# Kernel tuning notes

Measured on AMD Instinct MI355X. Metric: run time of the kernel, lower is better.

The kernel has to match this reference:

```python
import jax, jax.numpy as jnp
import numpy as np

B, N, C, H, K = 4, 16384, 256, 8, 64
D = C // H
EPS = 1e-8

def setup_inputs() -> dict:
    key = jax.random.key(0)
    ks = jax.random.split(key, 6)
    scale = 0.02
    return {
        "voxel_features": jax.random.normal(ks[0], (B, N, C), dtype=jnp.float32),
        "cluster_assignments": jax.random.uniform(ks[1], (B, N, K), dtype=jnp.float32),
        "w_qkv": jax.random.normal(ks[2], (C, 3 * C), dtype=jnp.float32) * scale,
        "w_proj": jax.random.normal(ks[3], (C, C), dtype=jnp.float32) * scale,
        "b_proj": jnp.zeros((C,), dtype=jnp.float32),
        "cluster_bias": jax.random.normal(ks[4], (K, K), dtype=jnp.float32) * scale,
    }

def reference(voxel_features, cluster_assignments, w_qkv, w_proj, b_proj, cluster_bias):
    b, n, c = voxel_features.shape
    h, d = H, c // H
    A = cluster_assignments                                  # (B,N,K)
    qkv = (voxel_features @ w_qkv).reshape(b, n, 3, h, d)    # (B,N,3,H,D)
    q = jnp.moveaxis(qkv[:, :, 0], 1, 2)                     # (B,H,N,D)
    k = jnp.moveaxis(qkv[:, :, 1], 1, 2)
    v = jnp.moveaxis(qkv[:, :, 2], 1, 2)
    # cluster mass per (batch, cluster)
    denom = A.sum(axis=1) + EPS                              # (B,K)
    # cluster-pooled K/V: contraction over N (the huge broadcast-sum in torch)
    k_cluster = jnp.einsum('bnk,bhnd->bhkd', A, k) / denom[:, None, :, None]
    v_cluster = jnp.einsum('bnk,bhnd->bhkd', A, v) / denom[:, None, :, None]
    attn = jnp.einsum('bhnd,bhkd->bhnk', q, k_cluster) * (d ** -0.5)
    bias = jnp.einsum('bnk,kl->bnl', A, cluster_bias)        # (B,N,K)
    attn = jax.nn.softmax(attn + bias[:, None, :, :], axis=-1)
    x = jnp.einsum('bhnk,bhkd->bhnd', attn, v_cluster)       # (B,H,N,D)
    x = jnp.moveaxis(x, 1, 2).reshape(b, n, c)               # (B,N,C)
    return x @ w_proj + b_proj
```

## Files before the change

### kernel.cpp

```cpp
#include <hip/hip_runtime.h>

#define NTOK 16384
#define BATCH 4

typedef __attribute__((ext_vector_type(8))) short bf16x8;
typedef __attribute__((ext_vector_type(8))) unsigned short ushort8;
typedef __attribute__((ext_vector_type(4))) float f32x4;

__device__ __forceinline__ unsigned short f2bf(float f) {
  union { float f; unsigned int u; } c; c.f = f;
  unsigned int r = c.u + 0x7fff + ((c.u >> 16) & 1);
  return (unsigned short)(r >> 16);
}

__device__ __forceinline__ float exp2_fast(float x) {
  float r;
  asm("v_exp_f32 %0, %1" : "=v"(r) : "v"(x));
  return r;
}

__global__ __launch_bounds__(256) void convall(const float* __restrict__ voxel,
                                               const float* __restrict__ A,
                                               const float* __restrict__ w_qkv,
                                               const float* __restrict__ w_proj,
                                               const float* __restrict__ cb,
                                               unsigned short* __restrict__ xb,
                                               unsigned short* __restrict__ Ab,
                                               unsigned short* __restrict__ wqT,
                                               unsigned short* __restrict__ wpT,
                                               unsigned short* __restrict__ cbbT) {
  const int blk = blockIdx.x;
  const int k = threadIdx.x;
  if (blk < 2048) {
    for (int i = blk * 256 + k; i < 2621440; i += 2048 * 256) {
      const float* src; unsigned short* dst; int j;
      if (i < 2097152) { j = i; src = voxel; dst = xb; }
      else { j = i - 2097152; src = A; dst = Ab; }
      float4 a = *(const float4*)(src + 8 * (size_t)j);
      float4 b = *(const float4*)(src + 8 * (size_t)j + 4);
      ushort8 o;
      o[0] = f2bf(a.x); o[1] = f2bf(a.y); o[2] = f2bf(a.z); o[3] = f2bf(a.w);
      o[4] = f2bf(b.x); o[5] = f2bf(b.y); o[6] = f2bf(b.z); o[7] = f2bf(b.w);
      *(ushort8*)(dst + 8 * (size_t)j) = o;
    }
  } else {
    int n = blk - 2048;
    if (n < 256) wqT[n * 256 + k] = f2bf(w_qkv[(size_t)k * 768 + n]);
    else if (n < 512) wpT[(n - 256) * 256 + k] = f2bf(w_proj[(size_t)k * 256 + (n - 256)]);
    else if (k < 64) {
      for (int j = 0; j < 64; ++j)
        cbbT[k * 64 + j] = f2bf(cb[j * 64 + k] * 1.4426950408889634f);
    }
  }
}

template <int ADD_BIAS, int C_BF16>
__global__ __launch_bounds__(256, 3) void gemm_mfma(const unsigned short* __restrict__ Ab,
                                                    const unsigned short* __restrict__ BT,
                                                    const float* __restrict__ bias,
                                                    void* __restrict__ Cv,
                                                    int N, int K, int lda) {
  __shared__ __align__(16) unsigned short smem[2][128][72];
  const int tid = threadIdx.x;
  int bx, by;
  if ((gridDim.y & 7) == 0) {
    int flat = blockIdx.y * gridDim.x + blockIdx.x;
    int xc = flat & 7, t = flat >> 3;
    int gx = gridDim.x, ypx = gridDim.y >> 3;
    bx = t % gx; by = xc * ypx + t / gx;
  } else { bx = blockIdx.x; by = blockIdx.y; }
  const int bn = bx * 128, bm = by * 128;
  const int lane = tid & 63;
  const int wv = tid >> 6;
  const int wm = wv & 1, wn = wv >> 1;
  const int m16 = lane & 15, quad = lane >> 4;

  const int srow = tid >> 1;
  const int scol = (tid & 1) * 32;

  const unsigned short* ga = Ab + (size_t)(bm + srow) * lda + scol;
  const unsigned short* gb = BT + (size_t)(bn + srow) * K + scol;

  ushort8 ra[2][4], rb[2][4];
#pragma unroll
  for (int kt = 0; kt < 2; ++kt)
#pragma unroll
    for (int i = 0; i < 4; ++i) {
      ra[kt][i] = *(const ushort8*)(ga + kt * 64 + 8 * i);
      rb[kt][i] = *(const ushort8*)(gb + kt * 64 + 8 * i);
    }

  f32x4 acc[4][4];
#pragma unroll
  for (int r = 0; r < 4; ++r)
#pragma unroll
    for (int c = 0; c < 4; ++c) acc[r][c] = (f32x4){0.f, 0.f, 0.f, 0.f};

#pragma unroll
  for (int kt = 0; kt < 4; ++kt) {
    const int sb = kt & 1;
    if (kt > 0) __syncthreads();
#pragma unroll
    for (int i = 0; i < 4; ++i) {
      *(ushort8*)&smem[0][srow][scol + 8 * i] = ra[sb][i];
      *(ushort8*)&smem[1][srow][scol + 8 * i] = rb[sb][i];
    }
    __syncthreads();
    if (kt < 2) {
#pragma unroll
      for (int i = 0; i < 4; ++i) {
        ra[sb][i] = *(const ushort8*)(ga + (kt + 2) * 64 + 8 * i);
        rb[sb][i] = *(const ushort8*)(gb + (kt + 2) * 64 + 8 * i);
      }
    }
#pragma unroll
    for (int ks = 0; ks < 64; ks += 32) {
      bf16x8 af[4], bf[4];
#pragma unroll
      for (int r = 0; r < 4; ++r)
        af[r] = *(const bf16x8*)&smem[0][wm * 64 + r * 16 + m16][ks + quad * 8];
#pragma unroll
      for (int c = 0; c < 4; ++c)
        bf[c] = *(const bf16x8*)&smem[1][wn * 64 + c * 16 + m16][ks + quad * 8];
#pragma unroll
      for (int r = 0; r < 4; ++r)
#pragma unroll
        for (int c = 0; c < 4; ++c)
          acc[r][c] = __builtin_amdgcn_mfma_f32_16x16x32_bf16(af[r], bf[c], acc[r][c], 0, 0, 0);
    }
  }

  float bv[4];
  if (ADD_BIAS) {
#pragma unroll
    for (int c = 0; c < 4; ++c) bv[c] = bias[bn + wn * 64 + c * 16 + m16];
  }
  const int lrD = tid >> 2, cch = (tid & 3) * 32;
  unsigned short* Csh = (unsigned short*)smem;
  float* Csf = (float*)smem;
#pragma unroll
  for (int p = 0; p < 2; ++p) {
    __syncthreads();
    if (wm == p) {
#pragma unroll
      for (int r = 0; r < 4; ++r) {
        int lr0 = r * 16 + quad * 4;
#pragma unroll
        for (int c = 0; c < 4; ++c) {
          int col = wn * 64 + c * 16 + m16;
#pragma unroll
          for (int i = 0; i < 4; ++i) {
            float v = acc[r][c][i] + (ADD_BIAS ? bv[c] : 0.f);
            if (C_BF16) Csh[(lr0 + i) * 136 + col] = f2bf(v);
            else Csf[(lr0 + i) * 132 + col] = v;
          }
        }
      }
    }
    __syncthreads();
    if (C_BF16) {
      unsigned short* gp = (unsigned short*)Cv + (size_t)(bm + p * 64 + lrD) * N + bn + cch;
      const unsigned short* sp = Csh + lrD * 136 + cch;
      ushort8 t0 = *(const ushort8*)(sp + 0);
      ushort8 t1 = *(const ushort8*)(sp + 8);
      ushort8 t2 = *(const ushort8*)(sp + 16);
      ushort8 t3 = *(const ushort8*)(sp + 24);
      *(ushort8*)(gp + 0) = t0;
      *(ushort8*)(gp + 8) = t1;
      *(ushort8*)(gp + 16) = t2;
      *(ushort8*)(gp + 24) = t3;
    } else {
      float* gp = (float*)Cv + (size_t)(bm + p * 64 + lrD) * N + bn + cch;
      const float* sp = Csf + lrD * 132 + cch;
      float4 t[8];
#pragma unroll
      for (int u = 0; u < 8; ++u) t[u] = *(const float4*)(sp + 4 * u);
#pragma unroll
      for (int u = 0; u < 8; ++u) *(float4*)(gp + 4 * u) = t[u];
    }
  }
}

__global__ __launch_bounds__(256) void pool_mfma(const unsigned short* __restrict__ Ab,
                                                 const unsigned short* __restrict__ xb,
                                                 float* __restrict__ part,
                                                 float* __restrict__ asump) {
  __shared__ unsigned short At[64][40];
  __shared__ unsigned short Xt[128][40];
  const int tid = threadIdx.x;
  const int tch = blockIdx.x, cblk = blockIdx.y, b = blockIdx.z;
  const int w = tid >> 6, lane = tid & 63;
  const int m16 = lane & 15, quad = lane >> 4;
  const size_t row0 = (size_t)b * NTOK + (size_t)tch * 256;
  const int cb0 = cblk * 128;
  const int tokL = tid & 31, gA = tid >> 5;

  f32x4 acc[4][2];
#pragma unroll
  for (int r = 0; r < 4; ++r)
#pragma unroll
    for (int c = 0; c < 2; ++c) acc[r][c] = (f32x4){0.f, 0.f, 0.f, 0.f};
  f32x4 acc1[4];
#pragma unroll
  for (int r = 0; r < 4; ++r) acc1[r] = (f32x4){0.f, 0.f, 0.f, 0.f};
  bf16x8 onesv;
#pragma unroll
  for (int i = 0; i < 8; ++i) onesv[i] = (short)0x3F80;

  ushort8 px[2], pa;
  auto loadG = [&](int t0) {
#pragma unroll
    for (int u = 0; u < 2; ++u) {
      int idx = tid + u * 256;
      int tok = idx & 31, g = idx >> 5;
      px[u] = *(const ushort8*)(xb + (row0 + t0 + tok) * 256 + cb0 + g * 8);
    }
    pa = *(const ushort8*)(Ab + (row0 + t0 + tokL) * 64 + gA * 8);
  };
  loadG(0);

  for (int ks = 0; ks < 8; ++ks) {
    __syncthreads();
#pragma unroll
    for (int u = 0; u < 2; ++u) {
      int idx = tid + u * 256;
      int tok = idx & 31, g = idx >> 5;
#pragma unroll
      for (int i = 0; i < 8; ++i) Xt[g * 8 + i][tok] = (unsigned short)px[u][i];
    }
#pragma unroll
    for (int i = 0; i < 8; ++i) At[gA * 8 + i][tokL] = (unsigned short)pa[i];
    __syncthreads();
    if (ks + 1 < 8) loadG((ks + 1) * 32);
    bf16x8 af[4], bfr[2];
#pragma unroll
    for (int r = 0; r < 4; ++r) af[r] = *(const bf16x8*)&At[r * 16 + m16][quad * 8];
#pragma unroll
    for (int c = 0; c < 2; ++c) bfr[c] = *(const bf16x8*)&Xt[w * 32 + c * 16 + m16][quad * 8];
#pragma unroll
    for (int r = 0; r < 4; ++r)
#pragma unroll
      for (int c = 0; c < 2; ++c)
        acc[r][c] = __builtin_amdgcn_mfma_f32_16x16x32_bf16(af[r], bfr[c], acc[r][c], 0, 0, 0);
    if (cblk == 0) {
#pragma unroll
      for (int r = 0; r < 4; ++r)
        acc1[r] = __builtin_amdgcn_mfma_f32_16x16x32_bf16(af[r], onesv, acc1[r], 0, 0, 0);
    }
  }

  float* pp = part + ((size_t)(b * 64 + tch) * 64) * 256 + cb0;
#pragma unroll
  for (int r = 0; r < 4; ++r)
#pragma unroll
    for (int c = 0; c < 2; ++c)
#pragma unroll
      for (int i = 0; i < 4; ++i) {
        int cl = r * 16 + quad * 4 + i;
        int ch = w * 32 + c * 16 + m16;
        pp[(size_t)cl * 256 + ch] = acc[r][c][i];
      }
  if (cblk == 0 && tid < 64 && m16 == 0) {
    float* ap = asump + ((size_t)(b * 64 + tch)) * 64;
#pragma unroll
    for (int r = 0; r < 4; ++r)
#pragma unroll
      for (int i = 0; i < 4; ++i)
        ap[r * 16 + quad * 4 + i] = acc1[r][i];
  }
}

__global__ __launch_bounds__(256) void pool2kv(const float* __restrict__ part,
                                               const float* __restrict__ asump,
                                               const float* __restrict__ w_qkv,
                                               unsigned short* __restrict__ kcb,
                                               unsigned short* __restrict__ vcbT) {
  __shared__ float px[256];
  __shared__ float dsh;
  const int bc = blockIdx.x;
  const int b = bc >> 6, cl = bc & 63;
  const int c = threadIdx.x;
  if (c < 64) {
    float av = asump[((size_t)(b * 64) + c) * 64 + cl];
#pragma unroll
    for (int msk = 1; msk < 64; msk <<= 1) av += __shfl_xor(av, msk);
    if (c == 0) dsh = av + 1e-8f;
  }
  const float* pp = part + ((size_t)(b * 64) * 64 + cl) * 256 + c;
  float s = 0.f;
#pragma unroll 4
  for (int t = 0; t < 64; ++t) s += pp[(size_t)t * 16384];
  px[c] = s;
  __syncthreads();
  float accK = 0.f, accV = 0.f;
#pragma unroll 8
  for (int k = 0; k < 256; ++k) {
    float x = px[k];
    accK = fmaf(x, w_qkv[(size_t)k * 768 + 256 + c], accK);
    accV = fmaf(x, w_qkv[(size_t)k * 768 + 512 + c], accV);
  }
  float inv = 1.f / dsh;
  int h = c >> 5, d = c & 31;
  kcb[(((size_t)b * 8 + h) * 64 + cl) * 32 + d] =
      f2bf(accK * inv * (0.17677669529663687f * 1.4426950408889634f));
  vcbT[(((size_t)b * 8 + h) * 32 + d) * 64 + cl] = f2bf(accV * inv);
}

__global__ __launch_bounds__(256, 2) void attn_mfma(const unsigned short* __restrict__ Ab,
                                                    const unsigned short* __restrict__ qb,
                                                    unsigned short* __restrict__ xout,
                                                    const unsigned short* __restrict__ kcb,
                                                    const unsigned short* __restrict__ vcbT,
                                                    const unsigned short* __restrict__ cbbT) {
  __shared__ __align__(16) unsigned short PA[64 * 72];
  __shared__ __align__(16) unsigned short XO[64 * 36];

  const int tid = threadIdx.x;
  const int nb = blockIdx.x, hq = blockIdx.y, b = blockIdx.z;
  const int h0 = hq * 4;
  const int w = tid >> 6, lane = tid & 63;
  const int m16 = lane & 15, quad = lane >> 4;
  const size_t row0 = (size_t)b * NTOK + (size_t)nb * 64;
  const int rA = w * 16 + m16;
  const size_t bh8 = (size_t)b * 8;
  const int l4 = lane >> 2, s3 = lane & 3;

  bf16x8 aA[2], cbf[2][4];
  bf16x8 qf[4], kcf[4][4], vtf[4][2][2];
#pragma unroll
  for (int ks = 0; ks < 2; ++ks)
    aA[ks] = *(const bf16x8*)(Ab + (row0 + rA) * 64 + ks * 32 + quad * 8);
#pragma unroll
  for (int hh = 0; hh < 4; ++hh)
    qf[hh] = *(const bf16x8*)(qb + (row0 + rA) * 256 + (h0 + hh) * 32 + quad * 8);
#pragma unroll
  for (int hh = 0; hh < 4; ++hh)
#pragma unroll
    for (int nt = 0; nt < 4; ++nt)
      kcf[hh][nt] = *(const bf16x8*)(kcb + ((bh8 + h0 + hh) * 64 + nt * 16 + m16) * 32 +
                                     quad * 8);
#pragma unroll
  for (int hh = 0; hh < 4; ++hh)
#pragma unroll
    for (int nt2 = 0; nt2 < 2; ++nt2)
#pragma unroll
      for (int kc2 = 0; kc2 < 2; ++kc2)
        vtf[hh][nt2][kc2] = *(const bf16x8*)(vcbT + ((bh8 + h0 + hh) * 32 + nt2 * 16 + m16) * 64 +
                                             kc2 * 32 + quad * 8);
#pragma unroll
  for (int ks = 0; ks < 2; ++ks)
#pragma unroll
    for (int nt = 0; nt < 4; ++nt)
      cbf[ks][nt] = *(const bf16x8*)(cbbT + (nt * 16 + m16) * 64 + ks * 32 + quad * 8);

  f32x4 bacc[4];
#pragma unroll
  for (int nt = 0; nt < 4; ++nt) bacc[nt] = (f32x4){0.f, 0.f, 0.f, 0.f};
#pragma unroll
  for (int ks = 0; ks < 2; ++ks)
#pragma unroll
    for (int nt = 0; nt < 4; ++nt)
      bacc[nt] = __builtin_amdgcn_mfma_f32_16x16x32_bf16(aA[ks], cbf[ks][nt], bacc[nt], 0, 0, 0);

#pragma unroll
  for (int hh = 0; hh < 4; ++hh) {
    const int h = h0 + hh;

    f32x4 acc[4];
#pragma unroll
    for (int nt = 0; nt < 4; ++nt)
      acc[nt] = __builtin_amdgcn_mfma_f32_16x16x32_bf16(qf[hh], kcf[hh][nt], bacc[nt], 0, 0, 0);

    f32x4 mxv, sv;
#pragma unroll
    for (int i = 0; i < 4; ++i)
      mxv[i] = fmaxf(fmaxf(acc[0][i], acc[1][i]), fmaxf(acc[2][i], acc[3][i]));
#pragma unroll
    for (int msk = 1; msk < 16; msk <<= 1)
#pragma unroll
      for (int i = 0; i < 4; ++i) mxv[i] = fmaxf(mxv[i], __shfl_xor(mxv[i], msk));
#pragma unroll
    for (int i = 0; i < 4; ++i) sv[i] = 0.f;
#pragma unroll
    for (int nt = 0; nt < 4; ++nt)
#pragma unroll
      for (int i = 0; i < 4; ++i) {
        float e = exp2_fast(acc[nt][i] - mxv[i]);
        acc[nt][i] = e;
        sv[i] += e;
      }
#pragma unroll
    for (int nt = 0; nt < 4; ++nt)
#pragma unroll
      for (int i = 0; i < 4; ++i)
        PA[(w * 16 + quad * 4 + i) * 72 + nt * 16 + m16] = f2bf(acc[nt][i]);
#pragma unroll
    for (int msk = 1; msk < 16; msk <<= 1)
#pragma unroll
      for (int i = 0; i < 4; ++i) sv[i] += __shfl_xor(sv[i], msk);
#pragma unroll
    for (int i = 0; i < 4; ++i) sv[i] = 1.f / sv[i];

    f32x4 acc2[2];
#pragma unroll
    for (int nt2 = 0; nt2 < 2; ++nt2) acc2[nt2] = (f32x4){0.f, 0.f, 0.f, 0.f};
#pragma unroll
    for (int kc2 = 0; kc2 < 2; ++kc2) {
      bf16x8 pf = *(const bf16x8*)&PA[rA * 72 + kc2 * 32 + quad * 8];
#pragma unroll
      for (int nt2 = 0; nt2 < 2; ++nt2)
        acc2[nt2] = __builtin_amdgcn_mfma_f32_16x16x32_bf16(pf, vtf[hh][nt2][kc2], acc2[nt2], 0, 0, 0);
    }

#pragma unroll
    for (int nt2 = 0; nt2 < 2; ++nt2)
#pragma unroll
      for (int i = 0; i < 4; ++i)
        XO[(w * 16 + quad * 4 + i) * 36 + nt2 * 16 + m16] = f2bf(acc2[nt2][i] * sv[i]);
    ushort8 xv = *(const ushort8*)&XO[(w * 16 + l4) * 36 + s3 * 8];
    *(ushort8*)(xout + (row0 + w * 16 + l4) * 256 + h * 32 + s3 * 8) = xv;
  }
}

extern "C" void kernel_launch(void* const* d_in, const int* in_sizes, int n_in,
                              void* d_out, int out_size, void* d_ws, size_t ws_size,
                              hipStream_t stream) {
  const float* voxel  = (const float*)d_in[0];
  const float* A      = (const float*)d_in[1];
  const float* w_qkv  = (const float*)d_in[2];
  const float* w_proj = (const float*)d_in[3];
  const float* b_proj = (const float*)d_in[4];
  const float* cb     = (const float*)d_in[5];
  float* out = (float*)d_out;
  (void)in_sizes; (void)n_in; (void)out_size; (void)ws_size;

  char* wsb = (char*)d_ws;
  unsigned short* qb       = (unsigned short*)wsb;
  unsigned short* xb       = (unsigned short*)(wsb + 33554432);
  float* part              = (float*)(wsb + 67108864);
  float* asump             = (float*)(wsb + 83886080);
  unsigned short* wqT      = (unsigned short*)(wsb + 83951616);
  unsigned short* wpT      = (unsigned short*)(wsb + 84082688);
  unsigned short* kcb      = (unsigned short*)(wsb + 84213760);
  unsigned short* vcbT     = (unsigned short*)(wsb + 84344832);
  unsigned short* cbbT     = (unsigned short*)(wsb + 84475904);
  unsigned short* Ab = (unsigned short*)d_out;

  convall<<<2561, 256, 0, stream>>>(voxel, A, w_qkv, w_proj, cb,
                                    xb, Ab, wqT, wpT, cbbT);

  gemm_mfma<0, 1><<<dim3(2, 512), 256, 0, stream>>>(xb, wqT, nullptr, qb,
                                                    256, 256, 256);

  pool_mfma<<<dim3(64, 2, BATCH), 256, 0, stream>>>(Ab, xb, part, asump);
  pool2kv<<<256, 256, 0, stream>>>(part, asump, w_qkv, kcb, vcbT);

  attn_mfma<<<dim3(NTOK / 64, 2, BATCH), 256, 0, stream>>>(Ab, qb, xb, kcb, vcbT, cbbT);

  gemm_mfma<1, 0><<<dim3(2, 512), 256, 0, stream>>>(xb, wpT, b_proj, out,
                                                    256, 256, 256);
}
```

Measured before the change: 265.6 us.

## Fuse Q projection GEMM into the cluster attention kernel

The separate Q GEMM kernel is removed, and its work moves into a new qattn kernel. Each block computes a 128x128 Q tile with MFMA, keeps it in LDS as bf16, then runs the cluster-bias, softmax and PV steps for its 4 heads and 128 tokens straight from shared memory. This drops the global write and re-read of the Q buffer and one kernel launch. The attention output now goes to the old Q buffer, which the projection GEMM (now a non-template kernel) reads. The trade-off is more LDS per block, which may lower occupancy, and attention tiles tied to the GEMM tile shape.

```diff
diff --git a/kernel.cpp b/kernel.cpp
--- a/kernel.cpp
+++ b/kernel.cpp
@@ -54,11 +54,10 @@
   }
 }
 
-template <int ADD_BIAS, int C_BF16>
-__global__ __launch_bounds__(256, 3) void gemm_mfma(const unsigned short* __restrict__ Ab,
+__global__ __launch_bounds__(256, 3) void gemm_proj(const unsigned short* __restrict__ Ab,
                                                     const unsigned short* __restrict__ BT,
                                                     const float* __restrict__ bias,
-                                                    void* __restrict__ Cv,
+                                                    float* __restrict__ Cv,
                                                     int N, int K, int lda) {
   __shared__ __align__(16) unsigned short smem[2][128][72];
   const int tid = threadIdx.x;
@@ -131,12 +130,9 @@
   }
 
   float bv[4];
-  if (ADD_BIAS) {
-#pragma unroll
-    for (int c = 0; c < 4; ++c) bv[c] = bias[bn + wn * 64 + c * 16 + m16];
-  }
+#pragma unroll
+  for (int c = 0; c < 4; ++c) bv[c] = bias[bn + wn * 64 + c * 16 + m16];
   const int lrD = tid >> 2, cch = (tid & 3) * 32;
-  unsigned short* Csh = (unsigned short*)smem;
   float* Csf = (float*)smem;
 #pragma unroll
   for (int p = 0; p < 2; ++p) {
@@ -149,35 +145,19 @@
         for (int c = 0; c < 4; ++c) {
           int col = wn * 64 + c * 16 + m16;
 #pragma unroll
-          for (int i = 0; i < 4; ++i) {
-            float v = acc[r][c][i] + (ADD_BIAS ? bv[c] : 0.f);
-            if (C_BF16) Csh[(lr0 + i) * 136 + col] = f2bf(v);
-            else Csf[(lr0 + i) * 132 + col] = v;
-          }
+          for (int i = 0; i < 4; ++i)
+            Csf[(lr0 + i) * 132 + col] = acc[r][c][i] + bv[c];
         }
       }
     }
     __syncthreads();
-    if (C_BF16) {
-      unsigned short* gp = (unsigned short*)Cv + (size_t)(bm + p * 64 + lrD) * N + bn + cch;
-      const unsigned short* sp = Csh + lrD * 136 + cch;
-      ushort8 t0 = *(const ushort8*)(sp + 0);
-      ushort8 t1 = *(const ushort8*)(sp + 8);
-      ushort8 t2 = *(const ushort8*)(sp + 16);
-      ushort8 t3 = *(const ushort8*)(sp + 24);
-      *(ushort8*)(gp + 0) = t0;
-      *(ushort8*)(gp + 8) = t1;
-      *(ushort8*)(gp + 16) = t2;
-      *(ushort8*)(gp + 24) = t3;
-    } else {
-      float* gp = (float*)Cv + (size_t)(bm + p * 64 + lrD) * N + bn + cch;
-      const float* sp = Csf + lrD * 132 + cch;
-      float4 t[8];
-#pragma unroll
-      for (int u = 0; u < 8; ++u) t[u] = *(const float4*)(sp + 4 * u);
-#pragma unroll
-      for (int u = 0; u < 8; ++u) *(float4*)(gp + 4 * u) = t[u];
-    }
+    float* gp = Cv + (size_t)(bm + p * 64 + lrD) * N + bn + cch;
+    const float* sp = Csf + lrD * 132 + cch;
+    float4 t[8];
+#pragma unroll
+    for (int u = 0; u < 8; ++u) t[u] = *(const float4*)(sp + 4 * u);
+#pragma unroll
+    for (int u = 0; u < 8; ++u) *(float4*)(gp + 4 * u) = t[u];
   }
 }
 
@@ -306,119 +286,223 @@
   vcbT[(((size_t)b * 8 + h) * 32 + d) * 64 + cl] = f2bf(accV * inv);
 }
 
-__global__ __launch_bounds__(256, 2) void attn_mfma(const unsigned short* __restrict__ Ab,
-                                                    const unsigned short* __restrict__ qb,
-                                                    unsigned short* __restrict__ xout,
-                                                    const unsigned short* __restrict__ kcb,
-                                                    const unsigned short* __restrict__ vcbT,
-                                                    const unsigned short* __restrict__ cbbT) {
-  __shared__ __align__(16) unsigned short PA[64 * 72];
-  __shared__ __align__(16) unsigned short XO[64 * 36];
+__global__ __launch_bounds__(256, 3) void qattn(const unsigned short* __restrict__ xb,
+                                                const unsigned short* __restrict__ wqT,
+                                                const unsigned short* __restrict__ Ab,
+                                                const unsigned short* __restrict__ kcb,
+                                                const unsigned short* __restrict__ vcbT,
+                                                const unsigned short* __restrict__ cbbT,
+                                                unsigned short* __restrict__ xout) {
+  __shared__ __align__(16) unsigned short smem[2][128][72];
+  __shared__ __align__(16) unsigned short Ps[128 * 68];
+  unsigned short* Qs = (unsigned short*)smem;
 
   const int tid = threadIdx.x;
-  const int nb = blockIdx.x, hq = blockIdx.y, b = blockIdx.z;
-  const int h0 = hq * 4;
-  const int w = tid >> 6, lane = tid & 63;
+  int bx, by;
+  {
+    int flat = blockIdx.y * gridDim.x + blockIdx.x;
+    int xc = flat & 7, t = flat >> 3;
+    int gx = gridDim.x, ypx = gridDim.y >> 3;
+    bx = t % gx; by = xc * ypx + t / gx;
+  }
+  const int bn = bx * 128, bm = by * 128;
+  const int lane = tid & 63;
+  const int wv = tid >> 6;
+  const int wm = wv & 1, wn = wv >> 1;
   const int m16 = lane & 15, quad = lane >> 4;
-  const size_t row0 = (size_t)b * NTOK + (size_t)nb * 64;
-  const int rA = w * 16 + m16;
+  const int srow = tid >> 1;
+  const int scol = (tid & 1) * 32;
+
+  const unsigned short* ga = xb + (size_t)(bm + srow) * 256 + scol;
+  const unsigned short* gb = wqT + (size_t)(bn + srow) * 256 + scol;
+
+  ushort8 ra[2][4], rb[2][4];
+#pragma unroll
+  for (int kt = 0; kt < 2; ++kt)
+#pragma unroll
+    for (int i = 0; i < 4; ++i) {
+      ra[kt][i] = *(const ushort8*)(ga + kt * 64 + 8 * i);
+      rb[kt][i] = *(const ushort8*)(gb + kt * 64 + 8 * i);
+    }
+
+  f32x4 acc[4][4];
+#pragma unroll
+  for (int r = 0; r < 4; ++r)
+#pragma unroll
+    for (int c = 0; c < 4; ++c) acc[r][c] = (f32x4){0.f, 0.f, 0.f, 0.f};
+
+#pragma unroll
+  for (int kt = 0; kt < 4; ++kt) {
+    const int sb = kt & 1;
+    if (kt > 0) __syncthreads();
+#pragma unroll
+    for (int i = 0; i < 4; ++i) {
+      *(ushort8*)&smem[0][srow][scol + 8 * i] = ra[sb][i];
+      *(ushort8*)&smem[1][srow][scol + 8 * i] = rb[sb][i];
+    }
+    __syncthreads();
+    if (kt < 2) {
+#pragma unroll
+      for (int i = 0; i < 4; ++i) {
+        ra[sb][i] = *(const ushort8*)(ga + (kt + 2) * 64 + 8 * i);
+        rb[sb][i] = *(const ushort8*)(gb + (kt + 2) * 64 + 8 * i);
+      }
+    }
+#pragma unroll
+    for (int ks = 0; ks < 64; ks += 32) {
+      bf16x8 af[4], bf[4];
+#pragma unroll
+      for (int r = 0; r < 4; ++r)
+        af[r] = *(const bf16x8*)&smem[0][wm * 64 + r * 16 + m16][ks + quad * 8];
+#pragma unroll
+      for (int c = 0; c < 4; ++c)
+        bf[c] = *(const bf16x8*)&smem[1][wn * 64 + c * 16 + m16][ks + quad * 8];
+#pragma unroll
+      for (int r = 0; r < 4; ++r)
+#pragma unroll
+        for (int c = 0; c < 4; ++c)
+          acc[r][c] = __builtin_amdgcn_mfma_f32_16x16x32_bf16(af[r], bf[c], acc[r][c], 0, 0, 0);
+    }
+  }
+
+  __syncthreads();
+#pragma unroll
+  for (int r = 0; r < 4; ++r) {
+    int lr0 = wm * 64 + r * 16 + quad * 4;
+#pragma unroll
+    for (int c = 0; c < 4; ++c) {
+      int col = wn * 64 + c * 16 + m16;
+#pragma unroll
+      for (int i = 0; i < 4; ++i)
+        Qs[(lr0 + i) * 132 + col] = f2bf(acc[r][c][i]);
+    }
+  }
+  __syncthreads();
+
+  const int w = wv;
+  const int b = bm >> 14;
   const size_t bh8 = (size_t)b * 8;
-  const int l4 = lane >> 2, s3 = lane & 3;
-
-  bf16x8 aA[2], cbf[2][4];
-  bf16x8 qf[4], kcf[4][4], vtf[4][2][2];
-#pragma unroll
-  for (int ks = 0; ks < 2; ++ks)
-    aA[ks] = *(const bf16x8*)(Ab + (row0 + rA) * 64 + ks * 32 + quad * 8);
-#pragma unroll
-  for (int hh = 0; hh < 4; ++hh)
-    qf[hh] = *(const bf16x8*)(qb + (row0 + rA) * 256 + (h0 + hh) * 32 + quad * 8);
-#pragma unroll
-  for (int hh = 0; hh < 4; ++hh)
+  const int h0 = bx * 4;
+  const int tr0 = w * 32;
+
+  f32x4 bacc[2][4];
+#pragma unroll
+  for (int rt = 0; rt < 2; ++rt)
+#pragma unroll
+    for (int nt = 0; nt < 4; ++nt) bacc[rt][nt] = (f32x4){0.f, 0.f, 0.f, 0.f};
+#pragma unroll
+  for (int ks = 0; ks < 2; ++ks) {
+    bf16x8 aA[2], cbf[4];
+#pragma unroll
+    for (int rt = 0; rt < 2; ++rt)
+      aA[rt] = *(const bf16x8*)(Ab + (size_t)(bm + tr0 + rt * 16 + m16) * 64 +
+                                ks * 32 + quad * 8);
 #pragma unroll
     for (int nt = 0; nt < 4; ++nt)
-      kcf[hh][nt] = *(const bf16x8*)(kcb + ((bh8 + h0 + hh) * 64 + nt * 16 + m16) * 32 +
-                                     quad * 8);
-#pragma unroll
-  for (int hh = 0; hh < 4; ++hh)
-#pragma unroll
-    for (int nt2 = 0; nt2 < 2; ++nt2)
-#pragma unroll
-      for (int kc2 = 0; kc2 < 2; ++kc2)
-        vtf[hh][nt2][kc2] = *(const bf16x8*)(vcbT + ((bh8 + h0 + hh) * 32 + nt2 * 16 + m16) * 64 +
-                                             kc2 * 32 + quad * 8);
-#pragma unroll
-  for (int ks = 0; ks < 2; ++ks)
-#pragma unroll
-    for (int nt = 0; nt < 4; ++nt)
-      cbf[ks][nt] = *(const bf16x8*)(cbbT + (nt * 16 + m16) * 64 + ks * 32 + quad * 8);
-
-  f32x4 bacc[4];
-#pragma unroll
-  for (int nt = 0; nt < 4; ++nt) bacc[nt] = (f32x4){0.f, 0.f, 0.f, 0.f};
-#pragma unroll
-  for (int ks = 0; ks < 2; ++ks)
-#pragma unroll
-    for (int nt = 0; nt < 4; ++nt)
-      bacc[nt] = __builtin_amdgcn_mfma_f32_16x16x32_bf16(aA[ks], cbf[ks][nt], bacc[nt], 0, 0, 0);
+      cbf[nt] = *(const bf16x8*)(cbbT + (nt * 16 + m16) * 64 + ks * 32 + quad * 8);
+#pragma unroll
+    for (int rt = 0; rt < 2; ++rt)
+#pragma unroll
+      for (int nt = 0; nt < 4; ++nt)
+        bacc[rt][nt] = __builtin_amdgcn_mfma_f32_16x16x32_bf16(aA[rt], cbf[nt], bacc[rt][nt], 0, 0, 0);
+  }
 
 #pragma unroll
   for (int hh = 0; hh < 4; ++hh) {
     const int h = h0 + hh;
 
-    f32x4 acc[4];
+    bf16x8 qf[2];
+#pragma unroll
+    for (int rt = 0; rt < 2; ++rt)
+      qf[rt] = *(const bf16x8*)&Qs[(tr0 + rt * 16 + m16) * 132 + hh * 32 + quad * 8];
+    bf16x8 kcf[4];
 #pragma unroll
     for (int nt = 0; nt < 4; ++nt)
-      acc[nt] = __builtin_amdgcn_mfma_f32_16x16x32_bf16(qf[hh], kcf[hh][nt], bacc[nt], 0, 0, 0);
-
-    f32x4 mxv, sv;
-#pragma unroll
-    for (int i = 0; i < 4; ++i)
-      mxv[i] = fmaxf(fmaxf(acc[0][i], acc[1][i]), fmaxf(acc[2][i], acc[3][i]));
-#pragma unroll
-    for (int msk = 1; msk < 16; msk <<= 1)
-#pragma unroll
-      for (int i = 0; i < 4; ++i) mxv[i] = fmaxf(mxv[i], __shfl_xor(mxv[i], msk));
-#pragma unroll
-    for (int i = 0; i < 4; ++i) sv[i] = 0.f;
-#pragma unroll
-    for (int nt = 0; nt < 4; ++nt)
-#pragma unroll
-      for (int i = 0; i < 4; ++i) {
-        float e = exp2_fast(acc[nt][i] - mxv[i]);
-        acc[nt][i] = e;
-        sv[i] += e;
-      }
-#pragma unroll
-    for (int nt = 0; nt < 4; ++nt)
+      kcf[nt] = *(const bf16x8*)(kcb + ((bh8 + h) * 64 + nt * 16 + m16) * 32 + quad * 8);
+    bf16x8 vtf[2][2];
+#pragma unroll
+    for (int nt2 = 0; nt2 < 2; ++nt2)
+#pragma unroll
+      for (int kc2 = 0; kc2 < 2; ++kc2)
+        vtf[nt2][kc2] = *(const bf16x8*)(vcbT + ((bh8 + h) * 32 + nt2 * 16 + m16) * 64 +
+                                         kc2 * 32 + quad * 8);
+
+    f32x4 sacc[2][4];
+#pragma unroll
+    for (int rt = 0; rt < 2; ++rt)
+#pragma unroll
+      for (int nt = 0; nt < 4; ++nt)
+        sacc[rt][nt] = __builtin_amdgcn_mfma_f32_16x16x32_bf16(qf[rt], kcf[nt], bacc[rt][nt], 0, 0, 0);
+
+    f32x4 svv[2];
+#pragma unroll
+    for (int rt = 0; rt < 2; ++rt) {
+      f32x4 mxv, sv;
 #pragma unroll
       for (int i = 0; i < 4; ++i)
-        PA[(w * 16 + quad * 4 + i) * 72 + nt * 16 + m16] = f2bf(acc[nt][i]);
-#pragma unroll
-    for (int msk = 1; msk < 16; msk <<= 1)
-#pragma unroll
-      for (int i = 0; i < 4; ++i) sv[i] += __shfl_xor(sv[i], msk);
-#pragma unroll
-    for (int i = 0; i < 4; ++i) sv[i] = 1.f / sv[i];
-
-    f32x4 acc2[2];
-#pragma unroll
-    for (int nt2 = 0; nt2 < 2; ++nt2) acc2[nt2] = (f32x4){0.f, 0.f, 0.f, 0.f};
+        mxv[i] = fmaxf(fmaxf(sacc[rt][0][i], sacc[rt][1][i]),
+                       fmaxf(sacc[rt][2][i], sacc[rt][3][i]));
+#pragma unroll
+      for (int msk = 1; msk < 16; msk <<= 1)
+#pragma unroll
+        for (int i = 0; i < 4; ++i) mxv[i] = fmaxf(mxv[i], __shfl_xor(mxv[i], msk));
+#pragma unroll
+      for (int i = 0; i < 4; ++i) sv[i] = 0.f;
+#pragma unroll
+      for (int nt = 0; nt < 4; ++nt)
+#pragma unroll
+        for (int i = 0; i < 4; ++i) {
+          float e = exp2_fast(sacc[rt][nt][i] - mxv[i]);
+          sacc[rt][nt][i] = e;
+          sv[i] += e;
+        }
+#pragma unroll
+      for (int nt = 0; nt < 4; ++nt)
+#pragma unroll
+        for (int i = 0; i < 4; ++i)
+          Ps[(tr0 + rt * 16 + quad * 4 + i) * 68 + nt * 16 + m16] = f2bf(sacc[rt][nt][i]);
+#pragma unroll
+      for (int msk = 1; msk < 16; msk <<= 1)
+#pragma unroll
+        for (int i = 0; i < 4; ++i) sv[i] += __shfl_xor(sv[i], msk);
+#pragma unroll
+      for (int i = 0; i < 4; ++i) svv[rt][i] = 1.f / sv[i];
+    }
+
+    f32x4 acc2[2][2];
+#pragma unroll
+    for (int rt = 0; rt < 2; ++rt)
+#pragma unroll
+      for (int nt2 = 0; nt2 < 2; ++nt2) acc2[rt][nt2] = (f32x4){0.f, 0.f, 0.f, 0.f};
 #pragma unroll
     for (int kc2 = 0; kc2 < 2; ++kc2) {
-      bf16x8 pf = *(const bf16x8*)&PA[rA * 72 + kc2 * 32 + quad * 8];
+      bf16x8 pf[2];
+#pragma unroll
+      for (int rt = 0; rt < 2; ++rt)
+        pf[rt] = *(const bf16x8*)&Ps[(tr0 + rt * 16 + m16) * 68 + kc2 * 32 + quad * 8];
+#pragma unroll
+      for (int rt = 0; rt < 2; ++rt)
+#pragma unroll
+        for (int nt2 = 0; nt2 < 2; ++nt2)
+          acc2[rt][nt2] = __builtin_amdgcn_mfma_f32_16x16x32_bf16(pf[rt], vtf[nt2][kc2], acc2[rt][nt2], 0, 0, 0);
+    }
+
+#pragma unroll
+    for (int rt = 0; rt < 2; ++rt)
 #pragma unroll
       for (int nt2 = 0; nt2 < 2; ++nt2)
-        acc2[nt2] = __builtin_amdgcn_mfma_f32_16x16x32_bf16(pf, vtf[hh][nt2][kc2], acc2[nt2], 0, 0, 0);
-    }
-
-#pragma unroll
-    for (int nt2 = 0; nt2 < 2; ++nt2)
-#pragma unroll
-      for (int i = 0; i < 4; ++i)
-        XO[(w * 16 + quad * 4 + i) * 36 + nt2 * 16 + m16] = f2bf(acc2[nt2][i] * sv[i]);
-    ushort8 xv = *(const ushort8*)&XO[(w * 16 + l4) * 36 + s3 * 8];
-    *(ushort8*)(xout + (row0 + w * 16 + l4) * 256 + h * 32 + s3 * 8) = xv;
+#pragma unroll
+        for (int i = 0; i < 4; ++i)
+          Ps[(tr0 + rt * 16 + quad * 4 + i) * 68 + nt2 * 16 + m16] =
+              f2bf(acc2[rt][nt2][i] * svv[rt][i]);
+    {
+      int rr = tr0 + (lane >> 1), sel = lane & 1;
+      ushort8 xv0 = *(const ushort8*)&Ps[rr * 68 + sel * 16];
+      ushort8 xv1 = *(const ushort8*)&Ps[rr * 68 + sel * 16 + 8];
+      unsigned short* gp = xout + (size_t)(bm + rr) * 256 + h * 32 + sel * 16;
+      *(ushort8*)gp = xv0;
+      *(ushort8*)(gp + 8) = xv1;
+    }
   }
 }
 
@@ -449,14 +533,11 @@
   convall<<<2561, 256, 0, stream>>>(voxel, A, w_qkv, w_proj, cb,
                                     xb, Ab, wqT, wpT, cbbT);
 
-  gemm_mfma<0, 1><<<dim3(2, 512), 256, 0, stream>>>(xb, wqT, nullptr, qb,
-                                                    256, 256, 256);
-
   pool_mfma<<<dim3(64, 2, BATCH), 256, 0, stream>>>(Ab, xb, part, asump);
   pool2kv<<<256, 256, 0, stream>>>(part, asump, w_qkv, kcb, vcbT);
 
-  attn_mfma<<<dim3(NTOK / 64, 2, BATCH), 256, 0, stream>>>(Ab, qb, xb, kcb, vcbT, cbbT);
-
-  gemm_mfma<1, 0><<<dim3(2, 512), 256, 0, stream>>>(xb, wpT, b_proj, out,
-                                                    256, 256, 256);
-}
+  qattn<<<dim3(2, 512), 256, 0, stream>>>(xb, wqT, Ab, kcb, vcbT, cbbT, qb);
+
+  gemm_proj<<<dim3(2, 512), 256, 0, stream>>>(qb, wpT, b_proj, out,
+                                              256, 256, 256);
+}
```

Measured after the change: 254.8 us. 4.1% less time.
